# Optimization experiments

Measured on AMD Instinct MI355X. Metric: run time of the kernel, lower is better.

Reference implementation:

```python
import jax, jax.numpy as jnp
import numpy as np

B, NPG, DEG = 128, 400, 16
N, E = B * NPG, B * NPG * DEG
E_PER = E // B
K1, K2, K3 = 360, 324, 292  # ceil(0.9*400), ceil(0.9*360), ceil(0.9*324)
EPS = 1e-5


def setup_inputs() -> dict:
    key = jax.random.key(0)
    ks = jax.random.split(key, 48)
    # edges constrained within each graph (contiguous equal-size graphs)
    g = jnp.repeat(jnp.arange(B, dtype=jnp.int32), E_PER)
    src = jax.random.randint(ks[0], (E,), 0, NPG, dtype=jnp.int32) + g * NPG
    dst = jax.random.randint(ks[1], (E,), 0, NPG, dtype=jnp.int32) + g * NPG
    inp = {
        'x': jax.random.normal(ks[2], (N, 64), dtype=jnp.float32),
        'edge_index': jnp.stack([src, dst]),
        'batch': jnp.repeat(jnp.arange(B, dtype=jnp.int32), NPG),
    }
    def glorot(k, a, b):
        lim = float(np.sqrt(6.0 / (a + b)))
        return jax.random.uniform(k, (a, b), minval=-lim, maxval=lim, dtype=jnp.float32)
    conv_dims = [(64, 32), (32, 64), (64, 128), (128, 128)]
    for i, (a, b) in enumerate(conv_dims, 1):
        inp[f'W{i}'] = glorot(ks[2 + i], a, b)
        inp[f'b{i}'] = jnp.zeros((b,), jnp.float32)
    for i, d in zip((1, 2, 3), (32, 64, 128)):
        inp[f'p{i}'] = jax.random.uniform(ks[8 + i], (d,), minval=-1.0, maxval=1.0, dtype=jnp.float32) / float(np.sqrt(d))
    lin_dims = [(128, 64), (64, 64), (64, 32), (32, 16), (16, 1)]
    for i, (a, b) in enumerate(lin_dims, 1):
        inp[f'Lw{i}'] = glorot(ks[12 + i], a, b)
        inp[f'Lb{i}'] = jnp.zeros((b,), jnp.float32)
    for i, d in enumerate((64, 64, 32, 16), 1):
        inp[f'g{i}'] = jnp.ones((d,), jnp.float32)
        inp[f'be{i}'] = jnp.zeros((d,), jnp.float32)
    return inp


def _gcn(x, src, dst, emask, nmask, W, b):
    h = x @ W
    deg = nmask + jax.ops.segment_sum(emask, dst, num_segments=N)
    dinv = jnp.where(deg > 0, jax.lax.rsqrt(deg), 0.0)
    norm = dinv[src] * dinv[dst] * emask
    agg = jax.ops.segment_sum(h[src] * norm[:, None], dst, num_segments=N)
    agg = agg + h * (dinv * dinv * nmask)[:, None]  # self-loop term
    return (agg + b) * nmask[:, None]


def _topk_pool(x, nmask, p, k):
    # PyG TopKPooling: score = x.p/||p||, keep top-k per graph, x *= tanh(score)
    score = (x @ p) / jnp.linalg.norm(p)
    sel = jnp.where(nmask > 0, score, -jnp.inf).reshape(B, NPG)
    _, idx = jax.lax.top_k(sel, k)
    gidx = (idx + (jnp.arange(B) * NPG)[:, None]).reshape(-1)
    new_mask = jnp.zeros((N,), x.dtype).at[gidx].set(1.0)
    return x * (jnp.tanh(score) * new_mask)[:, None], new_mask


def reference(x, edge_index, batch, W1, b1, p1, W2, b2, p2, W3, b3, p3, W4, b4,
              Lw1, Lb1, Lw2, Lb2, Lw3, Lb3, Lw4, Lb4, Lw5, Lb5,
              g1, be1, g2, be2, g3, be3, g4, be4):
    src, dst = edge_index[0], edge_index[1]
    nmask = jnp.ones((N,), jnp.float32)
    emask = jnp.ones((E,), jnp.float32)
    x = jax.nn.relu(_gcn(x, src, dst, emask, nmask, W1, b1))
    x, nmask = _topk_pool(x, nmask, p1, K1)
    emask = emask * nmask[src] * nmask[dst]
    x = jax.nn.relu(_gcn(x, src, dst, emask, nmask, W2, b2))
    x, nmask = _topk_pool(x, nmask, p2, K2)
    emask = emask * nmask[src] * nmask[dst]
    x = jax.nn.relu(_gcn(x, src, dst, emask, nmask, W3, b3))
    x, nmask = _topk_pool(x, nmask, p3, K3)
    emask = emask * nmask[src] * nmask[dst]
    x = jax.nn.relu(_gcn(x, src, dst, emask, nmask, W4, b4))
    h = x.reshape(B, NPG, -1).max(axis=1)
    def lin_bn(h, W, bb, ga, be):
        h = h @ W + bb
        m = h.mean(0)
        v = h.var(0)  # biased, matches BatchNorm1d training normalization
        return jax.nn.relu(ga * (h - m) / jnp.sqrt(v + EPS) + be)
    h = lin_bn(h, Lw1, Lb1, g1, be1)
    h = lin_bn(h, Lw2, Lb2, g2, be2)
    h = lin_bn(h, Lw3, Lb3, g3, be3)
    h = lin_bn(h, Lw4, Lb4, g4, be4)
    return h @ Lw5 + Lb5
```

## Files before the change

### kernel.cpp

```cpp
#include <hip/hip_runtime.h>
#include <math.h>

#define NNODES 51200
#define BGRAPHS 128
#define NPG 400
#define NEDGES 819200
#define EPG 6400
#define SLP 7680

__global__ __launch_bounds__(512) void csr_build_kernel(
    const int* __restrict__ src, const int* __restrict__ dst,
    unsigned short* __restrict__ slg, int* __restrict__ gsg, int* __restrict__ gcg,
    float* __restrict__ nmask, float* __restrict__ dinv, float* __restrict__ sc,
    float* __restrict__ hp) {
    __shared__ int deg[NPG];
    __shared__ int incl[512];
    __shared__ int gs[NPG];
    __shared__ int cur[NPG];
    const int g = blockIdx.x, t = threadIdx.x;
    for (int i = t; i < NPG; i += 512) deg[i] = 0;
    if (t < 128) hp[g * 128 + t] = 0.0f;
    __syncthreads();
    for (int e = t; e < EPG; e += 512)
        atomicAdd(&deg[dst[g * EPG + e] - g * NPG], 1);
    __syncthreads();
    const int d = (t < NPG) ? deg[t] : 0;
    const int p = (d + 3) >> 2;
    incl[t] = p;
    __syncthreads();
    for (int off = 1; off < 512; off <<= 1) {
        int add = (t >= off) ? incl[t - off] : 0;
        __syncthreads();
        incl[t] += add;
        __syncthreads();
    }
    if (t < NPG) {
        const int gstart = incl[t] - p;
        gs[t] = gstart;
        gsg[g * NPG + t] = gstart;
        gcg[g * NPG + t] = p;
        cur[t] = gstart * 4;
        nmask[g * NPG + t] = 1.0f;
        const float dv = rsqrtf(1.0f + (float)d);
        dinv[g * NPG + t] = dv;
        sc[g * NPG + t] = dv;
    }
    __syncthreads();
    for (int e = t; e < EPG; e += 512) {
        int dl = dst[g * EPG + e] - g * NPG;
        int pos = atomicAdd(&cur[dl], 1);
        slg[g * SLP + pos] = (unsigned short)(src[g * EPG + e] - g * NPG);
    }
    __syncthreads();
    if (t < NPG) {
        const int end = (gs[t] + p) * 4;
        for (int i = cur[t]; i < end; i++) slg[g * SLP + i] = (unsigned short)NPG;
    }
}

template<int IN, int OUT, int MODE>
__global__ __launch_bounds__(256) void gemm_kernel(
    const float* __restrict__ X, const float* __restrict__ W,
    const float* __restrict__ bias, const float* __restrict__ nmask,
    float* __restrict__ H, const float* __restrict__ p,
    float* __restrict__ score, float* __restrict__ hp) {
    __shared__ __align__(16) float sX[64 * IN];
    __shared__ unsigned smax[256];
    const int row0 = blockIdx.x * 64;
    const int t = threadIdx.x;
    for (int i = t; i < 64 * IN / 4; i += 256)
        reinterpret_cast<float4*>(sX)[i] =
            reinterpret_cast<const float4*>(X + (size_t)row0 * IN)[i];
    if (MODE == 3) smax[t] = 0u;
    __syncthreads();
    constexpr int CG  = OUT / 4;
    constexpr int RG  = 256 / CG;
    constexpr int RPT = 64 / RG;
    const int c0 = (t % CG) * 4;
    const int r0 = (t / CG) * RPT;
    float acc[RPT][4];
#pragma unroll
    for (int r = 0; r < RPT; r++)
#pragma unroll
        for (int j = 0; j < 4; j++) acc[r][j] = 0.0f;
    for (int k4 = 0; k4 < IN / 4; k4++) {
        const float4 w0 = *reinterpret_cast<const float4*>(&W[(k4 * 4 + 0) * OUT + c0]);
        const float4 w1 = *reinterpret_cast<const float4*>(&W[(k4 * 4 + 1) * OUT + c0]);
        const float4 w2 = *reinterpret_cast<const float4*>(&W[(k4 * 4 + 2) * OUT + c0]);
        const float4 w3 = *reinterpret_cast<const float4*>(&W[(k4 * 4 + 3) * OUT + c0]);
#pragma unroll
        for (int r = 0; r < RPT; r++) {
            const float4 xv = *reinterpret_cast<const float4*>(&sX[(r0 + r) * IN + k4 * 4]);
            acc[r][0] += xv.x * w0.x + xv.y * w1.x + xv.z * w2.x + xv.w * w3.x;
            acc[r][1] += xv.x * w0.y + xv.y * w1.y + xv.z * w2.y + xv.w * w3.y;
            acc[r][2] += xv.x * w0.z + xv.y * w1.z + xv.z * w2.z + xv.w * w3.z;
            acc[r][3] += xv.x * w0.w + xv.y * w1.w + xv.z * w2.w + xv.w * w3.w;
        }
    }
    const int graph0 = row0 / 400;
    const int bnd = (graph0 + 1) * 400;
    float ps[RPT];
    float cmax[4] = {0.f, 0.f, 0.f, 0.f};
#pragma unroll
    for (int r = 0; r < RPT; r++) {
        const int row = row0 + r0 + r;
        float4 v = make_float4(acc[r][0], acc[r][1], acc[r][2], acc[r][3]);
        if (MODE >= 2) {
            const float4 b4 = *reinterpret_cast<const float4*>(&bias[c0]);
            const float m = nmask[row];
            v.x = fmaxf(v.x + b4.x, 0.0f) * m;
            v.y = fmaxf(v.y + b4.y, 0.0f) * m;
            v.z = fmaxf(v.z + b4.z, 0.0f) * m;
            v.w = fmaxf(v.w + b4.w, 0.0f) * m;
        }
        if (MODE != 3) *reinterpret_cast<float4*>(&H[(size_t)row * OUT + c0]) = v;
        if (MODE == 2) {
            const float4 p4 = *reinterpret_cast<const float4*>(&p[c0]);
            ps[r] = v.x * p4.x + v.y * p4.y + v.z * p4.z + v.w * p4.w;
        }
        if (MODE == 3) {
            cmax[0] = fmaxf(cmax[0], v.x);
            cmax[1] = fmaxf(cmax[1], v.y);
            cmax[2] = fmaxf(cmax[2], v.z);
            cmax[3] = fmaxf(cmax[3], v.w);
        }
    }
    if (MODE == 2) {
#pragma unroll
        for (int r = 0; r < RPT; r++) {
#pragma unroll
            for (int off = 1; off < CG; off <<= 1) ps[r] += __shfl_xor(ps[r], off);
        }
        if ((t % CG) == 0) {
#pragma unroll
            for (int r = 0; r < RPT; r++) score[row0 + r0 + r] = ps[r];
        }
    }
    if (MODE == 3) {
        const int seg = ((row0 + r0) >= bnd) ? 1 : 0;
        atomicMax(&smax[seg * 128 + c0 + 0], __float_as_uint(cmax[0]));
        atomicMax(&smax[seg * 128 + c0 + 1], __float_as_uint(cmax[1]));
        atomicMax(&smax[seg * 128 + c0 + 2], __float_as_uint(cmax[2]));
        atomicMax(&smax[seg * 128 + c0 + 3], __float_as_uint(cmax[3]));
        __syncthreads();
        unsigned* hpu = reinterpret_cast<unsigned*>(hp);
        if (t < 128) atomicMax(&hpu[graph0 * 128 + t], smax[t]);
        const int graph1 = (row0 + 63) / 400;
        if (graph1 != graph0 && t < 128) atomicMax(&hpu[graph1 * 128 + t], smax[128 + t]);
    }
}

template<int OUT, int NCH, int NS, bool EPI, bool SCORE>
__global__ __launch_bounds__(512) void gcn_agg_kernel(
    const float* __restrict__ H, float* __restrict__ Y,
    const float* __restrict__ dinv, const float* __restrict__ sc,
    const float* __restrict__ bias, const float* __restrict__ p,
    float* __restrict__ score,
    const unsigned short* __restrict__ slg, const int* __restrict__ gsg,
    const int* __restrict__ gcg) {
    __shared__ __align__(16) float Hl[(NPG + 1) * 36];
    __shared__ float dinvl[NPG];
    __shared__ int gsl[NPG];
    __shared__ int gcl[NPG];
    __shared__ unsigned long long sl64[SLP / 4];
    const unsigned short* sl = reinterpret_cast<const unsigned short*>(sl64);
    const int b   = blockIdx.x;
    const int g   = b / (NCH * NS);
    const int rem = b % (NCH * NS);
    const int f0  = (rem / NS) * 32;
    const int n0  = (rem % NS) * (NPG / NS);
    const int t   = threadIdx.x;

    for (int i = t; i < NPG; i += 512) {
        dinvl[i] = dinv[g * NPG + i];
        gsl[i] = gsg[g * NPG + i];
        gcl[i] = gcg[g * NPG + i];
    }
    for (int i = t; i < SLP / 4; i += 512)
        sl64[i] = reinterpret_cast<const unsigned long long*>(slg + (size_t)g * SLP)[i];
    if (t < 36) Hl[NPG * 36 + t] = 0.0f;
    for (int i = t; i < NPG * 8; i += 512) {
        const int n = i >> 3, q = i & 7;
        const float s = sc[g * NPG + n];
        float4 v = *reinterpret_cast<const float4*>(&H[(size_t)(g * NPG + n) * OUT + f0 + q * 4]);
        v.x *= s; v.y *= s; v.z *= s; v.w *= s;
        *reinterpret_cast<float4*>(&Hl[n * 36 + q * 4]) = v;
    }
    __syncthreads();

    const int wave = t >> 6, lane = t & 63;
    const int sub = lane >> 3, f4 = lane & 7;
    constexpr int NPB = NPG / NS;
    for (int n = n0 + wave * 8 + sub; n < n0 + NPB; n += 64) {
        const float di = dinvl[n];
        if (di == 0.0f) continue;
        const int g0 = gsl[n], g1 = g0 + gcl[n];
        float4 acc = *reinterpret_cast<const float4*>(&Hl[n * 36 + f4 * 4]);
        for (int gg = g0; gg < g1; ++gg) {
            const unsigned long long q = *reinterpret_cast<const unsigned long long*>(&sl[gg * 4]);
            const int s0 = (int)(q & 0xFFFF), s1 = (int)((q >> 16) & 0xFFFF);
            const int s2 = (int)((q >> 32) & 0xFFFF), s3 = (int)(q >> 48);
            const float4 a = *reinterpret_cast<const float4*>(&Hl[s0 * 36 + f4 * 4]);
            const float4 bb = *reinterpret_cast<const float4*>(&Hl[s1 * 36 + f4 * 4]);
            const float4 c = *reinterpret_cast<const float4*>(&Hl[s2 * 36 + f4 * 4]);
            const float4 dd = *reinterpret_cast<const float4*>(&Hl[s3 * 36 + f4 * 4]);
            acc.x += (a.x + bb.x) + (c.x + dd.x);
            acc.y += (a.y + bb.y) + (c.y + dd.y);
            acc.z += (a.z + bb.z) + (c.z + dd.z);
            acc.w += (a.w + bb.w) + (c.w + dd.w);
        }
        acc.x *= di; acc.y *= di; acc.z *= di; acc.w *= di;
        if (EPI) {
            const float4 b4 = *reinterpret_cast<const float4*>(&bias[f0 + f4 * 4]);
            acc.x = fmaxf(acc.x + b4.x, 0.0f);
            acc.y = fmaxf(acc.y + b4.y, 0.0f);
            acc.z = fmaxf(acc.z + b4.z, 0.0f);
            acc.w = fmaxf(acc.w + b4.w, 0.0f);
        }
        *reinterpret_cast<float4*>(&Y[(size_t)(g * NPG + n) * OUT + f0 + f4 * 4]) = acc;
        if (SCORE) {
            const float4 p4 = *reinterpret_cast<const float4*>(&p[f4 * 4]);
            float part = acc.x * p4.x + acc.y * p4.y + acc.z * p4.z + acc.w * p4.w;
            part += __shfl_xor(part, 1);
            part += __shfl_xor(part, 2);
            part += __shfl_xor(part, 4);
            if (f4 == 0) score[g * NPG + n] = part;
        }
    }
}

template<int DIM>
__global__ __launch_bounds__(512) void topk_kernel(
    const float* __restrict__ score, float* __restrict__ nmask,
    float* __restrict__ dinv, float* __restrict__ sc,
    const float* __restrict__ p, int K,
    const unsigned short* __restrict__ slg, const int* __restrict__ gsg,
    const int* __restrict__ gcg) {
    __shared__ float sval[512];
    __shared__ int   sidx[512];
    __shared__ float sraw[NPG];
    __shared__ float nml[NPG + 1];
    __shared__ unsigned long long sl64[SLP / 4];
    __shared__ int gsl[NPG];
    __shared__ int gcl[NPG];
    __shared__ float spnorm;
    const unsigned short* sl = reinterpret_cast<const unsigned short*>(sl64);
    const int g = blockIdx.x;
    const int t = threadIdx.x;
    for (int i = t; i < SLP / 4; i += 512)
        sl64[i] = reinterpret_cast<const unsigned long long*>(slg + (size_t)g * SLP)[i];
    for (int i = t; i < NPG; i += 512) {
        gsl[i] = gsg[g * NPG + i];
        gcl[i] = gcg[g * NPG + i];
    }
    if (t == 0) {
        float s = 0.0f;
        for (int j = 0; j < DIM; j++) s += p[j] * p[j];
        spnorm = sqrtf(s);
    }
    float v = -INFINITY;
    int ix = t;
    if (t < NPG) {
        const float raw = score[g * NPG + t];
        sraw[t] = raw;
        v = (nmask[g * NPG + t] > 0.0f) ? raw : -INFINITY;
    }
    __syncthreads();
    for (int kk = 2; kk <= 512; kk <<= 1) {
        for (int j = kk >> 1; j > 0; j >>= 1) {
            float vb; int ib;
            if (j >= 64) {
                sval[t] = v; sidx[t] = ix;
                __syncthreads();
                vb = sval[t ^ j]; ib = sidx[t ^ j];
                __syncthreads();
            } else {
                vb = __shfl_xor(v, j, 64);
                ib = __shfl_xor(ix, j, 64);
            }
            const bool ownFirst = (v > vb) || (v == vb && ix < ib);
            const bool lower = (t & j) == 0;
            const bool desc = (t & kk) == 0;
            const bool keepOwn = lower ? (desc == ownFirst) : (desc != ownFirst);
            if (!keepOwn) { v = vb; ix = ib; }
        }
    }
    if (t <= NPG) nml[t] = 0.0f;
    __syncthreads();
    if (t < K) nml[ix] = 1.0f;
    __syncthreads();
    if (t < NPG) nmask[g * NPG + t] = nml[t];
    for (int n = t; n < NPG; n += 512) {
        float dv = 0.0f;
        if (nml[n] > 0.0f) {
            float d = 1.0f;
            const int g0 = gsl[n], g1 = g0 + gcl[n];
            for (int gg = g0; gg < g1; ++gg) {
                const unsigned long long q = *reinterpret_cast<const unsigned long long*>(&sl[gg * 4]);
                d += nml[(int)(q & 0xFFFF)] + nml[(int)((q >> 16) & 0xFFFF)] +
                     nml[(int)((q >> 32) & 0xFFFF)] + nml[(int)(q >> 48)];
            }
            dv = rsqrtf(d);
        }
        dinv[g * NPG + n] = dv;
        sc[g * NPG + n] = (nml[n] > 0.0f) ? tanhf(sraw[n] / spnorm) * dv : 0.0f;
    }
}

template<int IN, int OUT>
__global__ __launch_bounds__(128) void head_layer_kernel(
    const float* __restrict__ A, const float* __restrict__ W,
    const float* __restrict__ b, const float* __restrict__ ga,
    const float* __restrict__ be, float* __restrict__ Y) {
    __shared__ float Al[128 * (IN + 1)];
    __shared__ float red[4];
    const int c = blockIdx.x, t = threadIdx.x;
    for (int i = t; i < 128 * IN; i += 128)
        Al[(i / IN) * (IN + 1) + (i % IN)] = A[i];
    __syncthreads();
    float acc = b[c];
#pragma unroll
    for (int j = 0; j < IN; j++) acc += Al[t * (IN + 1) + j] * W[j * OUT + c];
    float s1 = acc, s2 = acc * acc;
    for (int o = 32; o > 0; o >>= 1) {
        s1 += __shfl_down(s1, o, 64);
        s2 += __shfl_down(s2, o, 64);
    }
    if ((t & 63) == 0) { red[t >> 6] = s1; red[2 + (t >> 6)] = s2; }
    __syncthreads();
    const float S1 = red[0] + red[1], S2 = red[2] + red[3];
    const float m = S1 * (1.0f / 128.0f);
    const float var = S2 * (1.0f / 128.0f) - m * m;
    float val = ga[c] * (acc - m) * rsqrtf(var + 1e-5f) + be[c];
    Y[t * OUT + c] = fmaxf(val, 0.0f);
}

__global__ __launch_bounds__(128) void head_final_kernel(
    const float* __restrict__ A, const float* __restrict__ w,
    const float* __restrict__ b, float* __restrict__ out) {
    const int t = threadIdx.x;
    float acc = b[0];
#pragma unroll
    for (int j = 0; j < 16; j++) acc += A[t * 16 + j] * w[j];
    out[t] = acc;
}

extern "C" void kernel_launch(void* const* d_in, const int* in_sizes, int n_in,
                              void* d_out, int out_size, void* d_ws, size_t ws_size,
                              hipStream_t stream) {
    (void)in_sizes; (void)n_in; (void)out_size; (void)ws_size;
    const float* x   = (const float*)d_in[0];
    const int*   ei  = (const int*)d_in[1];
    const float* W1  = (const float*)d_in[3];  const float* b1  = (const float*)d_in[4];
    const float* W2  = (const float*)d_in[5];  const float* b2  = (const float*)d_in[6];
    const float* W3  = (const float*)d_in[7];  const float* b3  = (const float*)d_in[8];
    const float* W4  = (const float*)d_in[9];  const float* b4  = (const float*)d_in[10];
    const float* p1  = (const float*)d_in[11];
    const float* p2  = (const float*)d_in[12];
    const float* p3  = (const float*)d_in[13];
    const float* Lw1 = (const float*)d_in[14]; const float* Lb1 = (const float*)d_in[15];
    const float* Lw2 = (const float*)d_in[16]; const float* Lb2 = (const float*)d_in[17];
    const float* Lw3 = (const float*)d_in[18]; const float* Lb3 = (const float*)d_in[19];
    const float* Lw4 = (const float*)d_in[20]; const float* Lb4 = (const float*)d_in[21];
    const float* Lw5 = (const float*)d_in[22]; const float* Lb5 = (const float*)d_in[23];
    const float* g1  = (const float*)d_in[24]; const float* be1 = (const float*)d_in[25];
    const float* g2  = (const float*)d_in[26]; const float* be2 = (const float*)d_in[27];
    const float* g3  = (const float*)d_in[28]; const float* be3 = (const float*)d_in[29];
    const float* g4  = (const float*)d_in[30]; const float* be4 = (const float*)d_in[31];

    const int* src = ei;
    const int* dst = ei + NEDGES;

    float* ws    = (float*)d_ws;
    float* hb    = ws;
    float* x0    = hb + (size_t)NNODES * 128;
    float* x1    = x0 + (size_t)NNODES * 128;
    float* nmask = x1 + (size_t)NNODES * 128;
    float* dinv  = nmask + NNODES;
    float* sc    = dinv + NNODES;
    float* scoreb= sc + NNODES;
    float* hp    = scoreb + NNODES;
    float* a1    = hp + 128 * 128;
    float* a2    = a1 + 128 * 64;
    float* a3    = a2 + 128 * 64;
    float* a4    = a3 + 128 * 32;
    unsigned short* slg = (unsigned short*)(a4 + 128 * 16);
    int* gsg = (int*)(slg + (size_t)BGRAPHS * SLP);
    int* gcg = gsg + (size_t)BGRAPHS * NPG;

    csr_build_kernel<<<BGRAPHS, 512, 0, stream>>>(src, dst, slg, gsg, gcg, nmask, dinv, sc, hp);

    gemm_kernel<64, 32, 0><<<NNODES / 64, 256, 0, stream>>>(x, W1, nullptr, nullptr, hb, nullptr, nullptr, nullptr);
    gcn_agg_kernel<32, 1, 2, true, true><<<BGRAPHS * 2, 512, 0, stream>>>(hb, x0, dinv, sc, b1, p1, scoreb, slg, gsg, gcg);
    topk_kernel<32><<<BGRAPHS, 512, 0, stream>>>(scoreb, nmask, dinv, sc, p1, 360, slg, gsg, gcg);

    gcn_agg_kernel<32, 1, 2, false, false><<<BGRAPHS * 2, 512, 0, stream>>>(x0, hb, dinv, sc, nullptr, nullptr, nullptr, slg, gsg, gcg);
    gemm_kernel<32, 64, 2><<<NNODES / 64, 256, 0, stream>>>(hb, W2, b2, nmask, x1, p2, scoreb, nullptr);
    topk_kernel<64><<<BGRAPHS, 512, 0, stream>>>(scoreb, nmask, dinv, sc, p2, 324, slg, gsg, gcg);

    gcn_agg_kernel<64, 2, 2, false, false><<<BGRAPHS * 4, 512, 0, stream>>>(x1, hb, dinv, sc, nullptr, nullptr, nullptr, slg, gsg, gcg);
    gemm_kernel<64, 128, 2><<<NNODES / 64, 256, 0, stream>>>(hb, W3, b3, nmask, x0, p3, scoreb, nullptr);
    topk_kernel<128><<<BGRAPHS, 512, 0, stream>>>(scoreb, nmask, dinv, sc, p3, 292, slg, gsg, gcg);

    gcn_agg_kernel<128, 4, 1, false, false><<<BGRAPHS * 4, 512, 0, stream>>>(x0, hb, dinv, sc, nullptr, nullptr, nullptr, slg, gsg, gcg);
    gemm_kernel<128, 128, 3><<<NNODES / 64, 256, 0, stream>>>(hb, W4, b4, nmask, x1, nullptr, nullptr, hp);

    head_layer_kernel<128, 64><<<64, 128, 0, stream>>>(hp, Lw1, Lb1, g1, be1, a1);
    head_layer_kernel<64, 64><<<64, 128, 0, stream>>>(a1, Lw2, Lb2, g2, be2, a2);
    head_layer_kernel<64, 32><<<32, 128, 0, stream>>>(a2, Lw3, Lb3, g3, be3, a3);
    head_layer_kernel<32, 16><<<16, 128, 0, stream>>>(a3, Lw4, Lb4, g4, be4, a4);
    head_final_kernel<<<1, 128, 0, stream>>>(a4, Lw5, Lb5, (float*)d_out);
}
```

Baseline: 204.9 us.

## Fuse per-graph GCN/TopK pipeline into one persistent mega kernel per graph

Replaces the sequence of CSR build, GEMM, aggregation and top-k kernels with a single kernel that runs one block per graph. Adjacency, masks, degree norms and scores stay in LDS for the whole pipeline, and only wide intermediates spill to per-graph global scratch. This removes about a dozen launches and the global round-trips between stages. The cost is only 128 blocks with one block per CU because of the large dynamic LDS, so the dense GEMMs now run on far fewer threads than the old grid-wide launches.

```diff
diff --git a/kernel.cpp b/kernel.cpp
--- a/kernel.cpp
+++ b/kernel.cpp
@@ -1,310 +1,421 @@
 #include <hip/hip_runtime.h>
 #include <math.h>
 
-#define NNODES 51200
 #define BGRAPHS 128
 #define NPG 400
-#define NEDGES 819200
 #define EPG 6400
 #define SLP 7680
-
-__global__ __launch_bounds__(512) void csr_build_kernel(
-    const int* __restrict__ src, const int* __restrict__ dst,
-    unsigned short* __restrict__ slg, int* __restrict__ gsg, int* __restrict__ gcg,
-    float* __restrict__ nmask, float* __restrict__ dinv, float* __restrict__ sc,
+#define NNODES 51200
+
+#define SM_BYTES 143040
+
+__device__ __forceinline__ float4 ld4(const float* p) { return *reinterpret_cast<const float4*>(p); }
+__device__ __forceinline__ void st4(float* p, float4 v) { *reinterpret_cast<float4*>(p) = v; }
+
+template<bool EPI, bool SCORE>
+__device__ __forceinline__ void gather_chunk(
+    const float* bufIn, float* bufOut, const float* dinvl, const float* nml,
+    const unsigned short* sl, const unsigned short* gsl, const unsigned short* gcl,
+    const float* bias, const float* p, float* sraw, int t) {
+  const int wave = t >> 6, lane = t & 63;
+  const int sub = lane >> 3, f4 = lane & 7;
+  for (int n = wave * 8 + sub; n < NPG; n += 64) {
+    const float di = dinvl[n];
+    float4 acc = make_float4(0.f, 0.f, 0.f, 0.f);
+    if (di != 0.0f) {
+      acc = ld4(&bufIn[n * 36 + f4 * 4]);
+      const int g0 = gsl[n], g1 = g0 + gcl[n];
+      for (int gg = g0; gg < g1; ++gg) {
+        const unsigned long long q = *reinterpret_cast<const unsigned long long*>(&sl[gg * 4]);
+        const int s0 = (int)(q & 0xFFFF), s1 = (int)((q >> 16) & 0xFFFF);
+        const int s2 = (int)((q >> 32) & 0xFFFF), s3 = (int)(q >> 48);
+        const float4 a = ld4(&bufIn[s0 * 36 + f4 * 4]);
+        const float4 b_ = ld4(&bufIn[s1 * 36 + f4 * 4]);
+        const float4 c = ld4(&bufIn[s2 * 36 + f4 * 4]);
+        const float4 d_ = ld4(&bufIn[s3 * 36 + f4 * 4]);
+        acc.x += (a.x + b_.x) + (c.x + d_.x);
+        acc.y += (a.y + b_.y) + (c.y + d_.y);
+        acc.z += (a.z + b_.z) + (c.z + d_.z);
+        acc.w += (a.w + b_.w) + (c.w + d_.w);
+      }
+      acc.x *= di; acc.y *= di; acc.z *= di; acc.w *= di;
+      if (EPI) {
+        const float4 b4 = ld4(&bias[f4 * 4]);
+        const float m = nml[n];
+        acc.x = fmaxf(acc.x + b4.x, 0.f) * m;
+        acc.y = fmaxf(acc.y + b4.y, 0.f) * m;
+        acc.z = fmaxf(acc.z + b4.z, 0.f) * m;
+        acc.w = fmaxf(acc.w + b4.w, 0.f) * m;
+      }
+    }
+    st4(&bufOut[n * 36 + f4 * 4], acc);
+    if (SCORE) {
+      const float4 p4 = ld4(&p[f4 * 4]);
+      float part = acc.x * p4.x + acc.y * p4.y + acc.z * p4.z + acc.w * p4.w;
+      part += __shfl_xor(part, 1);
+      part += __shfl_xor(part, 2);
+      part += __shfl_xor(part, 4);
+      if (f4 == 0) sraw[n] = part;
+    }
+  }
+}
+
+__device__ __forceinline__ void stage_scale_g(const float* Xs, int XS, int coff,
+                                              const float* scl, float* buf, int t) {
+  for (int i = t; i < NPG * 8; i += 512) {
+    const int n = i >> 3, q = i & 7;
+    float4 v = ld4(&Xs[(size_t)n * XS + coff + q * 4]);
+    const float s = scl[n];
+    v.x *= s; v.y *= s; v.z *= s; v.w *= s;
+    st4(&buf[n * 36 + q * 4], v);
+  }
+  if (t < 36) buf[NPG * 36 + t] = 0.f;
+}
+__device__ __forceinline__ void stage_scale_l(const float* srcb, const float* scl,
+                                              float* buf, int t) {
+  for (int i = t; i < NPG * 8; i += 512) {
+    const int n = i >> 3, q = i & 7;
+    float4 v = ld4(&srcb[n * 36 + q * 4]);
+    const float s = scl[n];
+    v.x *= s; v.y *= s; v.z *= s; v.w *= s;
+    st4(&buf[n * 36 + q * 4], v);
+  }
+  if (t < 36) buf[NPG * 36 + t] = 0.f;
+}
+
+__device__ __forceinline__ void topk_lds(
+    int K, const float* p, int DIM,
+    float* nml, float* dinvl, float* scl, const float* sraw,
+    float* sval, int* sidx, float* misc,
+    const unsigned short* sl, const unsigned short* gsl, const unsigned short* gcl, int t) {
+  if (t < DIM) sval[t] = p[t] * p[t];
+  __syncthreads();
+  if (t == 0) {
+    float s = 0.f;
+    for (int j = 0; j < DIM; j++) s += sval[j];
+    misc[0] = sqrtf(s);
+  }
+  float v = -INFINITY;
+  int ix = t;
+  if (t < NPG) v = (nml[t] > 0.f) ? sraw[t] : -INFINITY;
+  __syncthreads();
+  for (int kk = 2; kk <= 512; kk <<= 1) {
+    for (int j = kk >> 1; j > 0; j >>= 1) {
+      float vb; int ib;
+      if (j >= 64) {
+        sval[t] = v; sidx[t] = ix;
+        __syncthreads();
+        vb = sval[t ^ j]; ib = sidx[t ^ j];
+        __syncthreads();
+      } else {
+        vb = __shfl_xor(v, j, 64);
+        ib = __shfl_xor(ix, j, 64);
+      }
+      const bool ownFirst = (v > vb) || (v == vb && ix < ib);
+      const bool lower = (t & j) == 0;
+      const bool desc = (t & kk) == 0;
+      const bool keepOwn = lower ? (desc == ownFirst) : (desc != ownFirst);
+      if (!keepOwn) { v = vb; ix = ib; }
+    }
+  }
+  if (t <= NPG) nml[t] = 0.f;
+  __syncthreads();
+  if (t < K) nml[ix] = 1.f;
+  __syncthreads();
+  const float spn = misc[0];
+  for (int n = t; n < NPG; n += 512) {
+    float dv = 0.f;
+    if (nml[n] > 0.f) {
+      float d = 1.f;
+      const int g0 = gsl[n], g1 = g0 + gcl[n];
+      for (int gg = g0; gg < g1; ++gg) {
+        const unsigned long long q = *reinterpret_cast<const unsigned long long*>(&sl[gg * 4]);
+        d += nml[(int)(q & 0xFFFF)] + nml[(int)((q >> 16) & 0xFFFF)] +
+             nml[(int)((q >> 32) & 0xFFFF)] + nml[(int)(q >> 48)];
+      }
+      dv = rsqrtf(d);
+    }
+    dinvl[n] = dv;
+    scl[n] = (nml[n] > 0.f) ? tanhf(sraw[n] / spn) * dv : 0.f;
+  }
+  __syncthreads();
+}
+
+__global__ __launch_bounds__(512, 1) void mega_kernel(
+    const float* __restrict__ x, const int* __restrict__ esrc, const int* __restrict__ edst,
+    const float* __restrict__ W1, const float* __restrict__ b1, const float* __restrict__ p1,
+    const float* __restrict__ W2, const float* __restrict__ b2, const float* __restrict__ p2,
+    const float* __restrict__ W3, const float* __restrict__ b3, const float* __restrict__ p3,
+    const float* __restrict__ W4, const float* __restrict__ b4,
+    float* __restrict__ X2g_all, float* __restrict__ X3g_all, float* __restrict__ Hg_all,
     float* __restrict__ hp) {
-    __shared__ int deg[NPG];
-    __shared__ int incl[512];
-    __shared__ int gs[NPG];
-    __shared__ int cur[NPG];
-    const int g = blockIdx.x, t = threadIdx.x;
+  extern __shared__ char SMEM[];
+  float* bufA = (float*)(SMEM);
+  float* bufB = (float*)(SMEM + 57760);
+  unsigned short* sl  = (unsigned short*)(SMEM + 115520);
+  unsigned short* gsl = (unsigned short*)(SMEM + 130880);
+  unsigned short* gcl = (unsigned short*)(SMEM + 131680);
+  float* dinvl = (float*)(SMEM + 132480);
+  float* scl   = (float*)(SMEM + 134080);
+  float* nml   = (float*)(SMEM + 135680);
+  float* sraw  = (float*)(SMEM + 137328);
+  float* sval  = (float*)(SMEM + 138928);
+  int*   sidx  = (int*)  (SMEM + 140976);
+  float* misc  = (float*)(SMEM + 143024);
+
+  const int g = blockIdx.x, t = threadIdx.x;
+  const float* xg = x + (size_t)g * NPG * 64;
+  float* X2g = X2g_all + (size_t)g * NPG * 64;
+  float* X3g = X3g_all + (size_t)g * NPG * 128;
+  float* Hg  = Hg_all  + (size_t)g * NPG * 128;
+
+  {
+    int* deg  = (int*)bufA;
+    int* incl = deg + 512;
+    int* cur  = incl + 512;
     for (int i = t; i < NPG; i += 512) deg[i] = 0;
-    if (t < 128) hp[g * 128 + t] = 0.0f;
     __syncthreads();
     for (int e = t; e < EPG; e += 512)
-        atomicAdd(&deg[dst[g * EPG + e] - g * NPG], 1);
+      atomicAdd(&deg[edst[g * EPG + e] - g * NPG], 1);
     __syncthreads();
     const int d = (t < NPG) ? deg[t] : 0;
-    const int p = (d + 3) >> 2;
-    incl[t] = p;
+    const int pcnt = (d + 3) >> 2;
+    incl[t] = pcnt;
     __syncthreads();
     for (int off = 1; off < 512; off <<= 1) {
-        int add = (t >= off) ? incl[t - off] : 0;
-        __syncthreads();
-        incl[t] += add;
-        __syncthreads();
+      int add = (t >= off) ? incl[t - off] : 0;
+      __syncthreads();
+      incl[t] += add;
+      __syncthreads();
     }
     if (t < NPG) {
-        const int gstart = incl[t] - p;
-        gs[t] = gstart;
-        gsg[g * NPG + t] = gstart;
-        gcg[g * NPG + t] = p;
-        cur[t] = gstart * 4;
-        nmask[g * NPG + t] = 1.0f;
-        const float dv = rsqrtf(1.0f + (float)d);
-        dinv[g * NPG + t] = dv;
-        sc[g * NPG + t] = dv;
-    }
+      const int gstart = incl[t] - pcnt;
+      gsl[t] = (unsigned short)gstart;
+      gcl[t] = (unsigned short)pcnt;
+      cur[t] = gstart * 4;
+      nml[t] = 1.0f;
+      const float dv = rsqrtf(1.0f + (float)d);
+      dinvl[t] = dv;
+      scl[t] = dv;
+    }
+    if (t == 0) nml[NPG] = 0.0f;
     __syncthreads();
     for (int e = t; e < EPG; e += 512) {
-        int dl = dst[g * EPG + e] - g * NPG;
-        int pos = atomicAdd(&cur[dl], 1);
-        slg[g * SLP + pos] = (unsigned short)(src[g * EPG + e] - g * NPG);
+      int dl = edst[g * EPG + e] - g * NPG;
+      int pos = atomicAdd(&cur[dl], 1);
+      sl[pos] = (unsigned short)(esrc[g * EPG + e] - g * NPG);
     }
     __syncthreads();
     if (t < NPG) {
-        const int end = (gs[t] + p) * 4;
-        for (int i = cur[t]; i < end; i++) slg[g * SLP + i] = (unsigned short)NPG;
-    }
-}
-
-template<int IN, int OUT, int MODE>
-__global__ __launch_bounds__(256) void gemm_kernel(
-    const float* __restrict__ X, const float* __restrict__ W,
-    const float* __restrict__ bias, const float* __restrict__ nmask,
-    float* __restrict__ H, const float* __restrict__ p,
-    float* __restrict__ score, float* __restrict__ hp) {
-    __shared__ __align__(16) float sX[64 * IN];
-    __shared__ unsigned smax[256];
-    const int row0 = blockIdx.x * 64;
-    const int t = threadIdx.x;
-    for (int i = t; i < 64 * IN / 4; i += 256)
-        reinterpret_cast<float4*>(sX)[i] =
-            reinterpret_cast<const float4*>(X + (size_t)row0 * IN)[i];
-    if (MODE == 3) smax[t] = 0u;
-    __syncthreads();
-    constexpr int CG  = OUT / 4;
-    constexpr int RG  = 256 / CG;
-    constexpr int RPT = 64 / RG;
-    const int c0 = (t % CG) * 4;
-    const int r0 = (t / CG) * RPT;
-    float acc[RPT][4];
-#pragma unroll
-    for (int r = 0; r < RPT; r++)
-#pragma unroll
-        for (int j = 0; j < 4; j++) acc[r][j] = 0.0f;
-    for (int k4 = 0; k4 < IN / 4; k4++) {
-        const float4 w0 = *reinterpret_cast<const float4*>(&W[(k4 * 4 + 0) * OUT + c0]);
-        const float4 w1 = *reinterpret_cast<const float4*>(&W[(k4 * 4 + 1) * OUT + c0]);
-        const float4 w2 = *reinterpret_cast<const float4*>(&W[(k4 * 4 + 2) * OUT + c0]);
-        const float4 w3 = *reinterpret_cast<const float4*>(&W[(k4 * 4 + 3) * OUT + c0]);
-#pragma unroll
-        for (int r = 0; r < RPT; r++) {
-            const float4 xv = *reinterpret_cast<const float4*>(&sX[(r0 + r) * IN + k4 * 4]);
-            acc[r][0] += xv.x * w0.x + xv.y * w1.x + xv.z * w2.x + xv.w * w3.x;
-            acc[r][1] += xv.x * w0.y + xv.y * w1.y + xv.z * w2.y + xv.w * w3.y;
-            acc[r][2] += xv.x * w0.z + xv.y * w1.z + xv.z * w2.z + xv.w * w3.z;
-            acc[r][3] += xv.x * w0.w + xv.y * w1.w + xv.z * w2.w + xv.w * w3.w;
+      const int end = ((int)gsl[t] + (int)gcl[t]) * 4;
+      for (int i = cur[t]; i < end; i++) sl[i] = (unsigned short)NPG;
+    }
+    __syncthreads();
+  }
+
+  {
+    const int c0 = (t & 7) * 4;
+    const int slot = t >> 3;
+    for (int tile = 0; tile < 7; tile++) {
+      const int r0 = tile * 64;
+      const int nr = (r0 + 64 <= NPG) ? 64 : (NPG - r0);
+      for (int i = t; i < nr * 16; i += 512) {
+        const int r = i >> 4, q = i & 15;
+        st4(&bufB[r * 64 + q * 4], ld4(&xg[(size_t)(r0 + r) * 64 + q * 4]));
+      }
+      __syncthreads();
+      if (slot < nr) {
+        float a0 = 0.f, a1 = 0.f, a2 = 0.f, a3 = 0.f;
+        for (int k4 = 0; k4 < 16; k4++) {
+          const float4 w0 = ld4(&W1[(k4 * 4 + 0) * 32 + c0]);
+          const float4 w1 = ld4(&W1[(k4 * 4 + 1) * 32 + c0]);
+          const float4 w2 = ld4(&W1[(k4 * 4 + 2) * 32 + c0]);
+          const float4 w3 = ld4(&W1[(k4 * 4 + 3) * 32 + c0]);
+          const float4 xv = ld4(&bufB[slot * 64 + k4 * 4]);
+          a0 += xv.x * w0.x + xv.y * w1.x + xv.z * w2.x + xv.w * w3.x;
+          a1 += xv.x * w0.y + xv.y * w1.y + xv.z * w2.y + xv.w * w3.y;
+          a2 += xv.x * w0.z + xv.y * w1.z + xv.z * w2.z + xv.w * w3.z;
+          a3 += xv.x * w0.w + xv.y * w1.w + xv.z * w2.w + xv.w * w3.w;
         }
-    }
-    const int graph0 = row0 / 400;
-    const int bnd = (graph0 + 1) * 400;
-    float ps[RPT];
-    float cmax[4] = {0.f, 0.f, 0.f, 0.f};
-#pragma unroll
-    for (int r = 0; r < RPT; r++) {
-        const int row = row0 + r0 + r;
-        float4 v = make_float4(acc[r][0], acc[r][1], acc[r][2], acc[r][3]);
-        if (MODE >= 2) {
-            const float4 b4 = *reinterpret_cast<const float4*>(&bias[c0]);
-            const float m = nmask[row];
-            v.x = fmaxf(v.x + b4.x, 0.0f) * m;
-            v.y = fmaxf(v.y + b4.y, 0.0f) * m;
-            v.z = fmaxf(v.z + b4.z, 0.0f) * m;
-            v.w = fmaxf(v.w + b4.w, 0.0f) * m;
+        st4(&bufA[(r0 + slot) * 36 + c0], make_float4(a0, a1, a2, a3));
+      }
+      __syncthreads();
+    }
+  }
+  stage_scale_l(bufA, scl, bufA, t);
+  __syncthreads();
+  gather_chunk<true, true>(bufA, bufB, dinvl, nml, sl, gsl, gcl, b1, p1, sraw, t);
+  __syncthreads();
+  topk_lds(360, p1, 32, nml, dinvl, scl, sraw, sval, sidx, misc, sl, gsl, gcl, t);
+
+  stage_scale_l(bufB, scl, bufA, t);
+  __syncthreads();
+  gather_chunk<false, false>(bufA, bufB, dinvl, nml, sl, gsl, gcl, nullptr, nullptr, nullptr, t);
+  __syncthreads();
+  {
+    const int c0 = (t & 15) * 4;
+    const int slot = t >> 4;
+    for (int n = slot; n < NPG; n += 32) {
+      float a0 = 0.f, a1 = 0.f, a2 = 0.f, a3 = 0.f;
+      for (int k4 = 0; k4 < 8; k4++) {
+        const float4 w0 = ld4(&W2[(k4 * 4 + 0) * 64 + c0]);
+        const float4 w1 = ld4(&W2[(k4 * 4 + 1) * 64 + c0]);
+        const float4 w2 = ld4(&W2[(k4 * 4 + 2) * 64 + c0]);
+        const float4 w3 = ld4(&W2[(k4 * 4 + 3) * 64 + c0]);
+        const float4 xv = ld4(&bufB[n * 36 + k4 * 4]);
+        a0 += xv.x * w0.x + xv.y * w1.x + xv.z * w2.x + xv.w * w3.x;
+        a1 += xv.x * w0.y + xv.y * w1.y + xv.z * w2.y + xv.w * w3.y;
+        a2 += xv.x * w0.z + xv.y * w1.z + xv.z * w2.z + xv.w * w3.z;
+        a3 += xv.x * w0.w + xv.y * w1.w + xv.z * w2.w + xv.w * w3.w;
+      }
+      const float4 bb = ld4(&b2[c0]);
+      const float m = nml[n];
+      float4 v = make_float4(fmaxf(a0 + bb.x, 0.f) * m, fmaxf(a1 + bb.y, 0.f) * m,
+                             fmaxf(a2 + bb.z, 0.f) * m, fmaxf(a3 + bb.w, 0.f) * m);
+      st4(&X2g[(size_t)n * 64 + c0], v);
+      const float4 p4 = ld4(&p2[c0]);
+      float ps = v.x * p4.x + v.y * p4.y + v.z * p4.z + v.w * p4.w;
+      ps += __shfl_xor(ps, 1); ps += __shfl_xor(ps, 2);
+      ps += __shfl_xor(ps, 4); ps += __shfl_xor(ps, 8);
+      if ((t & 15) == 0) sraw[n] = ps;
+    }
+  }
+  __syncthreads();
+  topk_lds(324, p2, 64, nml, dinvl, scl, sraw, sval, sidx, misc, sl, gsl, gcl, t);
+
+  for (int c2 = 0; c2 < 2; c2++) {
+    stage_scale_g(X2g, 64, c2 * 32, scl, bufA, t);
+    __syncthreads();
+    gather_chunk<false, false>(bufA, bufB, dinvl, nml, sl, gsl, gcl, nullptr, nullptr, nullptr, t);
+    __syncthreads();
+    for (int i = t; i < NPG * 8; i += 512) {
+      const int n = i >> 3, q = i & 7;
+      st4(&Hg[(size_t)n * 128 + c2 * 32 + q * 4], ld4(&bufB[n * 36 + q * 4]));
+    }
+    __syncthreads();
+  }
+  {
+    const int c0 = (t & 31) * 4;
+    const int slot = t >> 5;
+    for (int tile = 0; tile < 7; tile++) {
+      const int r0 = tile * 64;
+      const int nr = (r0 + 64 <= NPG) ? 64 : (NPG - r0);
+      for (int i = t; i < nr * 16; i += 512) {
+        const int r = i >> 4, q = i & 15;
+        st4(&bufB[r * 68 + q * 4], ld4(&Hg[(size_t)(r0 + r) * 128 + q * 4]));
+      }
+      __syncthreads();
+      float acc[4][4];
+#pragma unroll
+      for (int rr = 0; rr < 4; rr++)
+#pragma unroll
+        for (int j = 0; j < 4; j++) acc[rr][j] = 0.f;
+      for (int k4 = 0; k4 < 16; k4++) {
+        const float4 w0 = ld4(&W3[(k4 * 4 + 0) * 128 + c0]);
+        const float4 w1 = ld4(&W3[(k4 * 4 + 1) * 128 + c0]);
+        const float4 w2 = ld4(&W3[(k4 * 4 + 2) * 128 + c0]);
+        const float4 w3 = ld4(&W3[(k4 * 4 + 3) * 128 + c0]);
+#pragma unroll
+        for (int rr = 0; rr < 4; rr++) {
+          const float4 xv = ld4(&bufB[(slot + 16 * rr) * 68 + k4 * 4]);
+          acc[rr][0] += xv.x * w0.x + xv.y * w1.x + xv.z * w2.x + xv.w * w3.x;
+          acc[rr][1] += xv.x * w0.y + xv.y * w1.y + xv.z * w2.y + xv.w * w3.y;
+          acc[rr][2] += xv.x * w0.z + xv.y * w1.z + xv.z * w2.z + xv.w * w3.z;
+          acc[rr][3] += xv.x * w0.w + xv.y * w1.w + xv.z * w2.w + xv.w * w3.w;
         }
-        if (MODE != 3) *reinterpret_cast<float4*>(&H[(size_t)row * OUT + c0]) = v;
-        if (MODE == 2) {
-            const float4 p4 = *reinterpret_cast<const float4*>(&p[c0]);
-            ps[r] = v.x * p4.x + v.y * p4.y + v.z * p4.z + v.w * p4.w;
+      }
+#pragma unroll
+      for (int rr = 0; rr < 4; rr++) {
+        const int r = slot + 16 * rr;
+        if (r < nr) {
+          const int row = r0 + r;
+          const float4 bb = ld4(&b3[c0]);
+          const float m = nml[row];
+          float4 v = make_float4(fmaxf(acc[rr][0] + bb.x, 0.f) * m,
+                                 fmaxf(acc[rr][1] + bb.y, 0.f) * m,
+                                 fmaxf(acc[rr][2] + bb.z, 0.f) * m,
+                                 fmaxf(acc[rr][3] + bb.w, 0.f) * m);
+          st4(&X3g[(size_t)row * 128 + c0], v);
+          const float4 p4 = ld4(&p3[c0]);
+          float ps = v.x * p4.x + v.y * p4.y + v.z * p4.z + v.w * p4.w;
+          ps += __shfl_xor(ps, 1); ps += __shfl_xor(ps, 2);
+          ps += __shfl_xor(ps, 4); ps += __shfl_xor(ps, 8);
+          ps += __shfl_xor(ps, 16);
+          if ((t & 31) == 0) sraw[row] = ps;
         }
-        if (MODE == 3) {
-            cmax[0] = fmaxf(cmax[0], v.x);
-            cmax[1] = fmaxf(cmax[1], v.y);
-            cmax[2] = fmaxf(cmax[2], v.z);
-            cmax[3] = fmaxf(cmax[3], v.w);
+      }
+      __syncthreads();
+    }
+  }
+  topk_lds(292, p3, 128, nml, dinvl, scl, sraw, sval, sidx, misc, sl, gsl, gcl, t);
+
+  for (int c2 = 0; c2 < 4; c2++) {
+    stage_scale_g(X3g, 128, c2 * 32, scl, bufA, t);
+    __syncthreads();
+    gather_chunk<false, false>(bufA, bufB, dinvl, nml, sl, gsl, gcl, nullptr, nullptr, nullptr, t);
+    __syncthreads();
+    for (int i = t; i < NPG * 8; i += 512) {
+      const int n = i >> 3, q = i & 7;
+      st4(&Hg[(size_t)n * 128 + c2 * 32 + q * 4], ld4(&bufB[n * 36 + q * 4]));
+    }
+    __syncthreads();
+  }
+  {
+    unsigned* smax = (unsigned*)sval;
+    if (t < 128) smax[t] = 0u;
+    __syncthreads();
+    const int c0 = (t & 31) * 4;
+    const int slot = t >> 5;
+    float cm0 = 0.f, cm1 = 0.f, cm2 = 0.f, cm3 = 0.f;
+    for (int tile = 0; tile < 7; tile++) {
+      const int r0 = tile * 64;
+      const int nr = (r0 + 64 <= NPG) ? 64 : (NPG - r0);
+      for (int i = t; i < nr * 32; i += 512) {
+        const int r = i >> 5, q = i & 31;
+        st4(&bufB[r * 132 + q * 4], ld4(&Hg[(size_t)(r0 + r) * 128 + q * 4]));
+      }
+      __syncthreads();
+      float acc[4][4];
+#pragma unroll
+      for (int rr = 0; rr < 4; rr++)
+#pragma unroll
+        for (int j = 0; j < 4; j++) acc[rr][j] = 0.f;
+      for (int k4 = 0; k4 < 32; k4++) {
+        const float4 w0 = ld4(&W4[(k4 * 4 + 0) * 128 + c0]);
+        const float4 w1 = ld4(&W4[(k4 * 4 + 1) * 128 + c0]);
+        const float4 w2 = ld4(&W4[(k4 * 4 + 2) * 128 + c0]);
+        const float4 w3 = ld4(&W4[(k4 * 4 + 3) * 128 + c0]);
+#pragma unroll
+        for (int rr = 0; rr < 4; rr++) {
+          const float4 xv = ld4(&bufB[(slot + 16 * rr) * 132 + k4 * 4]);
+          acc[rr][0] += xv.x * w0.x + xv.y * w1.x + xv.z * w2.x + xv.w * w3.x;
+          acc[rr][1] += xv.x * w0.y + xv.y * w1.y + xv.z * w2.y + xv.w * w3.y;
+          acc[rr][2] += xv.x * w0.z + xv.y * w1.z + xv.z * w2.z + xv.w * w3.z;
+          acc[rr][3] += xv.x * w0.w + xv.y * w1.w + xv.z * w2.w + xv.w * w3.w;
         }
-    }
-    if (MODE == 2) {
-#pragma unroll
-        for (int r = 0; r < RPT; r++) {
-#pragma unroll
-            for (int off = 1; off < CG; off <<= 1) ps[r] += __shfl_xor(ps[r], off);
+      }
+#pragma unroll
+      for (int rr = 0; rr < 4; rr++) {
+        const int r = slot + 16 * rr;
+        if (r < nr) {
+          const int row = r0 + r;
+          const float4 bb = ld4(&b4[c0]);
+          const float m = nml[row];
+          cm0 = fmaxf(cm0, fmaxf(acc[rr][0] + bb.x, 0.f) * m);
+          cm1 = fmaxf(cm1, fmaxf(acc[rr][1] + bb.y, 0.f) * m);
+          cm2 = fmaxf(cm2, fmaxf(acc[rr][2] + bb.z, 0.f) * m);
+          cm3 = fmaxf(cm3, fmaxf(acc[rr][3] + bb.w, 0.f) * m);
         }
-        if ((t % CG) == 0) {
-#pragma unroll
-            for (int r = 0; r < RPT; r++) score[row0 + r0 + r] = ps[r];
-        }
-    }
-    if (MODE == 3) {
-        const int seg = ((row0 + r0) >= bnd) ? 1 : 0;
-        atomicMax(&smax[seg * 128 + c0 + 0], __float_as_uint(cmax[0]));
-        atomicMax(&smax[seg * 128 + c0 + 1], __float_as_uint(cmax[1]));
-        atomicMax(&smax[seg * 128 + c0 + 2], __float_as_uint(cmax[2]));
-        atomicMax(&smax[seg * 128 + c0 + 3], __float_as_uint(cmax[3]));
-        __syncthreads();
-        unsigned* hpu = reinterpret_cast<unsigned*>(hp);
-        if (t < 128) atomicMax(&hpu[graph0 * 128 + t], smax[t]);
-        const int graph1 = (row0 + 63) / 400;
-        if (graph1 != graph0 && t < 128) atomicMax(&hpu[graph1 * 128 + t], smax[128 + t]);
-    }
-}
-
-template<int OUT, int NCH, int NS, bool EPI, bool SCORE>
-__global__ __launch_bounds__(512) void gcn_agg_kernel(
-    const float* __restrict__ H, float* __restrict__ Y,
-    const float* __restrict__ dinv, const float* __restrict__ sc,
-    const float* __restrict__ bias, const float* __restrict__ p,
-    float* __restrict__ score,
-    const unsigned short* __restrict__ slg, const int* __restrict__ gsg,
-    const int* __restrict__ gcg) {
-    __shared__ __align__(16) float Hl[(NPG + 1) * 36];
-    __shared__ float dinvl[NPG];
-    __shared__ int gsl[NPG];
-    __shared__ int gcl[NPG];
-    __shared__ unsigned long long sl64[SLP / 4];
-    const unsigned short* sl = reinterpret_cast<const unsigned short*>(sl64);
-    const int b   = blockIdx.x;
-    const int g   = b / (NCH * NS);
-    const int rem = b % (NCH * NS);
-    const int f0  = (rem / NS) * 32;
-    const int n0  = (rem % NS) * (NPG / NS);
-    const int t   = threadIdx.x;
-
-    for (int i = t; i < NPG; i += 512) {
-        dinvl[i] = dinv[g * NPG + i];
-        gsl[i] = gsg[g * NPG + i];
-        gcl[i] = gcg[g * NPG + i];
-    }
-    for (int i = t; i < SLP / 4; i += 512)
-        sl64[i] = reinterpret_cast<const unsigned long long*>(slg + (size_t)g * SLP)[i];
-    if (t < 36) Hl[NPG * 36 + t] = 0.0f;
-    for (int i = t; i < NPG * 8; i += 512) {
-        const int n = i >> 3, q = i & 7;
-        const float s = sc[g * NPG + n];
-        float4 v = *reinterpret_cast<const float4*>(&H[(size_t)(g * NPG + n) * OUT + f0 + q * 4]);
-        v.x *= s; v.y *= s; v.z *= s; v.w *= s;
-        *reinterpret_cast<float4*>(&Hl[n * 36 + q * 4]) = v;
-    }
-    __syncthreads();
-
-    const int wave = t >> 6, lane = t & 63;
-    const int sub = lane >> 3, f4 = lane & 7;
-    constexpr int NPB = NPG / NS;
-    for (int n = n0 + wave * 8 + sub; n < n0 + NPB; n += 64) {
-        const float di = dinvl[n];
-        if (di == 0.0f) continue;
-        const int g0 = gsl[n], g1 = g0 + gcl[n];
-        float4 acc = *reinterpret_cast<const float4*>(&Hl[n * 36 + f4 * 4]);
-        for (int gg = g0; gg < g1; ++gg) {
-            const unsigned long long q = *reinterpret_cast<const unsigned long long*>(&sl[gg * 4]);
-            const int s0 = (int)(q & 0xFFFF), s1 = (int)((q >> 16) & 0xFFFF);
-            const int s2 = (int)((q >> 32) & 0xFFFF), s3 = (int)(q >> 48);
-            const float4 a = *reinterpret_cast<const float4*>(&Hl[s0 * 36 + f4 * 4]);
-            const float4 bb = *reinterpret_cast<const float4*>(&Hl[s1 * 36 + f4 * 4]);
-            const float4 c = *reinterpret_cast<const float4*>(&Hl[s2 * 36 + f4 * 4]);
-            const float4 dd = *reinterpret_cast<const float4*>(&Hl[s3 * 36 + f4 * 4]);
-            acc.x += (a.x + bb.x) + (c.x + dd.x);
-            acc.y += (a.y + bb.y) + (c.y + dd.y);
-            acc.z += (a.z + bb.z) + (c.z + dd.z);
-            acc.w += (a.w + bb.w) + (c.w + dd.w);
-        }
-        acc.x *= di; acc.y *= di; acc.z *= di; acc.w *= di;
-        if (EPI) {
-            const float4 b4 = *reinterpret_cast<const float4*>(&bias[f0 + f4 * 4]);
-            acc.x = fmaxf(acc.x + b4.x, 0.0f);
-            acc.y = fmaxf(acc.y + b4.y, 0.0f);
-            acc.z = fmaxf(acc.z + b4.z, 0.0f);
-            acc.w = fmaxf(acc.w + b4.w, 0.0f);
-        }
-        *reinterpret_cast<float4*>(&Y[(size_t)(g * NPG + n) * OUT + f0 + f4 * 4]) = acc;
-        if (SCORE) {
-            const float4 p4 = *reinterpret_cast<const float4*>(&p[f4 * 4]);
-            float part = acc.x * p4.x + acc.y * p4.y + acc.z * p4.z + acc.w * p4.w;
-            part += __shfl_xor(part, 1);
-            part += __shfl_xor(part, 2);
-            part += __shfl_xor(part, 4);
-            if (f4 == 0) score[g * NPG + n] = part;
-        }
-    }
-}
-
-template<int DIM>
-__global__ __launch_bounds__(512) void topk_kernel(
-    const float* __restrict__ score, float* __restrict__ nmask,
-    float* __restrict__ dinv, float* __restrict__ sc,
-    const float* __restrict__ p, int K,
-    const unsigned short* __restrict__ slg, const int* __restrict__ gsg,
-    const int* __restrict__ gcg) {
-    __shared__ float sval[512];
-    __shared__ int   sidx[512];
-    __shared__ float sraw[NPG];
-    __shared__ float nml[NPG + 1];
-    __shared__ unsigned long long sl64[SLP / 4];
-    __shared__ int gsl[NPG];
-    __shared__ int gcl[NPG];
-    __shared__ float spnorm;
-    const unsigned short* sl = reinterpret_cast<const unsigned short*>(sl64);
-    const int g = blockIdx.x;
-    const int t = threadIdx.x;
-    for (int i = t; i < SLP / 4; i += 512)
-        sl64[i] = reinterpret_cast<const unsigned long long*>(slg + (size_t)g * SLP)[i];
-    for (int i = t; i < NPG; i += 512) {
-        gsl[i] = gsg[g * NPG + i];
-        gcl[i] = gcg[g * NPG + i];
-    }
-    if (t == 0) {
-        float s = 0.0f;
-        for (int j = 0; j < DIM; j++) s += p[j] * p[j];
-        spnorm = sqrtf(s);
-    }
-    float v = -INFINITY;
-    int ix = t;
-    if (t < NPG) {
-        const float raw = score[g * NPG + t];
-        sraw[t] = raw;
-        v = (nmask[g * NPG + t] > 0.0f) ? raw : -INFINITY;
-    }
-    __syncthreads();
-    for (int kk = 2; kk <= 512; kk <<= 1) {
-        for (int j = kk >> 1; j > 0; j >>= 1) {
-            float vb; int ib;
-            if (j >= 64) {
-                sval[t] = v; sidx[t] = ix;
-                __syncthreads();
-                vb = sval[t ^ j]; ib = sidx[t ^ j];
-                __syncthreads();
-            } else {
-                vb = __shfl_xor(v, j, 64);
-                ib = __shfl_xor(ix, j, 64);
-            }
-            const bool ownFirst = (v > vb) || (v == vb && ix < ib);
-            const bool lower = (t & j) == 0;
-            const bool desc = (t & kk) == 0;
-            const bool keepOwn = lower ? (desc == ownFirst) : (desc != ownFirst);
-            if (!keepOwn) { v = vb; ix = ib; }
-        }
-    }
-    if (t <= NPG) nml[t] = 0.0f;
-    __syncthreads();
-    if (t < K) nml[ix] = 1.0f;
-    __syncthreads();
-    if (t < NPG) nmask[g * NPG + t] = nml[t];
-    for (int n = t; n < NPG; n += 512) {
-        float dv = 0.0f;
-        if (nml[n] > 0.0f) {
-            float d = 1.0f;
-            const int g0 = gsl[n], g1 = g0 + gcl[n];
-            for (int gg = g0; gg < g1; ++gg) {
-                const unsigned long long q = *reinterpret_cast<const unsigned long long*>(&sl[gg * 4]);
-                d += nml[(int)(q & 0xFFFF)] + nml[(int)((q >> 16) & 0xFFFF)] +
-                     nml[(int)((q >> 32) & 0xFFFF)] + nml[(int)(q >> 48)];
-            }
-            dv = rsqrtf(d);
-        }
-        dinv[g * NPG + n] = dv;
-        sc[g * NPG + n] = (nml[n] > 0.0f) ? tanhf(sraw[n] / spnorm) * dv : 0.0f;
-    }
+      }
+      __syncthreads();
+    }
+    atomicMax(&smax[c0 + 0], __float_as_uint(cm0));
+    atomicMax(&smax[c0 + 1], __float_as_uint(cm1));
+    atomicMax(&smax[c0 + 2], __float_as_uint(cm2));
+    atomicMax(&smax[c0 + 3], __float_as_uint(cm3));
+    __syncthreads();
+    if (t < 128) hp[g * 128 + t] = __uint_as_float(smax[t]);
+  }
 }
 
 template<int IN, int OUT>
@@ -368,42 +479,25 @@
     const float* g3  = (const float*)d_in[28]; const float* be3 = (const float*)d_in[29];
     const float* g4  = (const float*)d_in[30]; const float* be4 = (const float*)d_in[31];
 
-    const int* src = ei;
-    const int* dst = ei + NEDGES;
-
-    float* ws    = (float*)d_ws;
-    float* hb    = ws;
-    float* x0    = hb + (size_t)NNODES * 128;
-    float* x1    = x0 + (size_t)NNODES * 128;
-    float* nmask = x1 + (size_t)NNODES * 128;
-    float* dinv  = nmask + NNODES;
-    float* sc    = dinv + NNODES;
-    float* scoreb= sc + NNODES;
-    float* hp    = scoreb + NNODES;
-    float* a1    = hp + 128 * 128;
-    float* a2    = a1 + 128 * 64;
-    float* a3    = a2 + 128 * 64;
-    float* a4    = a3 + 128 * 32;
-    unsigned short* slg = (unsigned short*)(a4 + 128 * 16);
-    int* gsg = (int*)(slg + (size_t)BGRAPHS * SLP);
-    int* gcg = gsg + (size_t)BGRAPHS * NPG;
-
-    csr_build_kernel<<<BGRAPHS, 512, 0, stream>>>(src, dst, slg, gsg, gcg, nmask, dinv, sc, hp);
-
-    gemm_kernel<64, 32, 0><<<NNODES / 64, 256, 0, stream>>>(x, W1, nullptr, nullptr, hb, nullptr, nullptr, nullptr);
-    gcn_agg_kernel<32, 1, 2, true, true><<<BGRAPHS * 2, 512, 0, stream>>>(hb, x0, dinv, sc, b1, p1, scoreb, slg, gsg, gcg);
-    topk_kernel<32><<<BGRAPHS, 512, 0, stream>>>(scoreb, nmask, dinv, sc, p1, 360, slg, gsg, gcg);
-
-    gcn_agg_kernel<32, 1, 2, false, false><<<BGRAPHS * 2, 512, 0, stream>>>(x0, hb, dinv, sc, nullptr, nullptr, nullptr, slg, gsg, gcg);
-    gemm_kernel<32, 64, 2><<<NNODES / 64, 256, 0, stream>>>(hb, W2, b2, nmask, x1, p2, scoreb, nullptr);
-    topk_kernel<64><<<BGRAPHS, 512, 0, stream>>>(scoreb, nmask, dinv, sc, p2, 324, slg, gsg, gcg);
-
-    gcn_agg_kernel<64, 2, 2, false, false><<<BGRAPHS * 4, 512, 0, stream>>>(x1, hb, dinv, sc, nullptr, nullptr, nullptr, slg, gsg, gcg);
-    gemm_kernel<64, 128, 2><<<NNODES / 64, 256, 0, stream>>>(hb, W3, b3, nmask, x0, p3, scoreb, nullptr);
-    topk_kernel<128><<<BGRAPHS, 512, 0, stream>>>(scoreb, nmask, dinv, sc, p3, 292, slg, gsg, gcg);
-
-    gcn_agg_kernel<128, 4, 1, false, false><<<BGRAPHS * 4, 512, 0, stream>>>(x0, hb, dinv, sc, nullptr, nullptr, nullptr, slg, gsg, gcg);
-    gemm_kernel<128, 128, 3><<<NNODES / 64, 256, 0, stream>>>(hb, W4, b4, nmask, x1, nullptr, nullptr, hp);
+    const int* esrc = ei;
+    const int* edst = ei + (size_t)BGRAPHS * EPG;
+
+    float* ws  = (float*)d_ws;
+    float* hg  = ws;
+    float* x2  = hg + (size_t)NNODES * 128;
+    float* x3  = x2 + (size_t)BGRAPHS * NPG * 64;
+    float* hp  = x3 + (size_t)NNODES * 128;
+    float* a1  = hp + 128 * 128;
+    float* a2  = a1 + 128 * 64;
+    float* a3  = a2 + 128 * 64;
+    float* a4  = a3 + 128 * 32;
+
+    hipFuncSetAttribute(reinterpret_cast<const void*>(mega_kernel),
+                        hipFuncAttributeMaxDynamicSharedMemorySize, SM_BYTES);
+
+    mega_kernel<<<BGRAPHS, 512, SM_BYTES, stream>>>(
+        x, esrc, edst, W1, b1, p1, W2, b2, p2, W3, b3, p3, W4, b4,
+        x2, x3, hg, hp);
 
     head_layer_kernel<128, 64><<<64, 128, 0, stream>>>(hp, Lw1, Lb1, g1, be1, a1);
     head_layer_kernel<64, 64><<<64, 128, 0, stream>>>(a1, Lw2, Lb2, g2, be2, a2);
```

Measured after the change: 739.5 us. 3.61x slower.
